# Performance work log

Measured on AMD Instinct MI355X. Metric: run time of the kernel, lower is better.

## Reference

```python
import jax, jax.numpy as jnp
import numpy as np

N = 65536
H = 1024
E = 3  # experts: SwishGLU, GEGLU, ReGLU


def setup_inputs() -> dict:
    key = jax.random.key(0)
    ks = jax.random.split(key, 10)
    s = 1.0 / np.sqrt(H)
    return {
        "x": jax.random.normal(ks[0], (N, H), jnp.float32),
        "W1": jax.random.normal(ks[1], (E, H, H), jnp.float32) * s,
        "b1": jax.random.normal(ks[2], (E, H), jnp.float32) * s,
        "W2": jax.random.normal(ks[3], (E, H, H), jnp.float32) * s,
        "b2": jax.random.normal(ks[4], (E, H), jnp.float32) * s,
        "W3": jax.random.normal(ks[5], (E, H, H), jnp.float32) * s,
        "b3": jax.random.normal(ks[6], (E, H), jnp.float32) * s,
        "Wg": jax.random.normal(ks[7], (H, E), jnp.float32) * s,
        "bg": jax.random.normal(ks[8], (E,), jnp.float32) * s,
        "gumbel_u": jax.random.uniform(ks[9], (N, E), jnp.float32),
    }


def reference(x, W1, b1, W2, b2, W3, b3, Wg, bg, gumbel_u):
    # Gate: hard gumbel-softmax (tau=1, hard=True) with straight-through estimator
    logits = x @ Wg + bg                                   # [N, E]
    u = jnp.clip(gumbel_u, 1e-6, 1.0 - 1e-6)
    g = -jnp.log(-jnp.log(u))                              # Gumbel(0,1) noise
    y_soft = jax.nn.softmax(logits + g, axis=-1)           # [N, E]
    y_hard = jax.nn.one_hot(jnp.argmax(y_soft, axis=-1), E, dtype=x.dtype)
    gate = y_hard + y_soft - jax.lax.stop_gradient(y_soft)  # values == y_hard

    # Dense compute of all three GLU experts (faithful to original module)
    h1 = jnp.einsum('nd,edh->enh', x, W1) + b1[:, None, :]  # [E, N, H]
    h3 = jnp.einsum('nd,edh->enh', x, W3) + b3[:, None, :]  # [E, N, H]
    acts = jnp.stack([
        jax.nn.silu(h1[0]),                       # SwishGLU
        jax.nn.gelu(h1[1], approximate=False),    # GEGLU (exact erf gelu)
        jax.nn.relu(h1[2]),                       # ReGLU
    ], axis=0)                                    # [E, N, H]
    inner = acts * h3                             # [E, N, H]
    out_e = jnp.einsum('end,edh->enh', inner, W2) + b2[:, None, :]  # [E, N, H]

    # Select/mix with (hard) gate weights
    return jnp.einsum('enh,ne->nh', out_e, gate)  # [N, H]
```

## Files before the change

### kernel.cpp

```cpp
#include <hip/hip_runtime.h>
#include <math.h>

#define N_TOK 65536
#define H_DIM 1024

typedef __attribute__((ext_vector_type(8))) short bf16x8;
typedef __attribute__((ext_vector_type(4))) float f32x4;

static const size_t WS_CNT   = 0;
static const size_t WS_OFFS  = 64;
static const size_t WS_PERM  = 128;
static const size_t WS_WT1   = 1ull << 20;
static const size_t WS_WT3   = WS_WT1 + 6291456ull;
static const size_t WS_WT2   = WS_WT3 + 6291456ull;
static const size_t WS_XB    = 20ull << 20;
static const size_t WS_INNER = WS_XB + 134217728ull;

static __device__ __forceinline__ unsigned short f2bf(float f) {
  union { float f; unsigned int u; } v; v.f = f;
  unsigned int r = v.u + 0x7fffu + ((v.u >> 16) & 1u);
  return (unsigned short)(r >> 16);
}

__global__ void init_kernel(int* cnt) {
  if (threadIdx.x < 4) cnt[threadIdx.x] = 0;
}

__global__ __launch_bounds__(1024) void gate_kernel(
    const float* __restrict__ x, const float* __restrict__ Wg,
    const float* __restrict__ bg, const float* __restrict__ gu,
    unsigned short* __restrict__ xb, int* __restrict__ cnt,
    int* __restrict__ perm)
{
  __shared__ float wg[3072];
  __shared__ int bexp[16];
  for (int i = threadIdx.x; i < 3072; i += 1024) wg[i] = Wg[i];
  __syncthreads();
  const int wave = threadIdx.x >> 6;
  const int lane = threadIdx.x & 63;
  const int n0 = blockIdx.x * 16;
  const int n = n0 + wave;
  const float4* xrow = (const float4*)(x + (size_t)n * H_DIM);
  unsigned short* xbrow = xb + (size_t)n * H_DIM;
  float s0 = 0.f, s1 = 0.f, s2 = 0.f;
#pragma unroll
  for (int j = 0; j < 4; j++) {
    float4 v = xrow[j * 64 + lane];
    int d0 = (j * 64 + lane) * 4;
    const float* w = &wg[d0 * 3];
    s0 += v.x * w[0] + v.y * w[3] + v.z * w[6] + v.w * w[9];
    s1 += v.x * w[1] + v.y * w[4] + v.z * w[7] + v.w * w[10];
    s2 += v.x * w[2] + v.y * w[5] + v.z * w[8] + v.w * w[11];
    uint2 p;
    p.x = (unsigned)f2bf(v.x) | ((unsigned)f2bf(v.y) << 16);
    p.y = (unsigned)f2bf(v.z) | ((unsigned)f2bf(v.w) << 16);
    ((uint2*)xbrow)[j * 64 + lane] = p;
  }
#pragma unroll
  for (int o = 32; o; o >>= 1) {
    s0 += __shfl_xor(s0, o);
    s1 += __shfl_xor(s1, o);
    s2 += __shfl_xor(s2, o);
  }
  if (lane == 0) {
    const float* u = gu + (size_t)n * 3;
    float l[3] = { s0 + bg[0], s1 + bg[1], s2 + bg[2] };
    int best = 0; float bs = -1e30f;
#pragma unroll
    for (int e = 0; e < 3; e++) {
      float uc = fminf(fmaxf(u[e], 1e-6f), 1.f - 1e-6f);
      float g = -logf(-logf(uc));
      float s = l[e] + g;
      if (s > bs) { bs = s; best = e; }
    }
    bexp[wave] = best;
  }
  __syncthreads();
  if (threadIdx.x == 0) {
    int lc[3] = {0, 0, 0};
    int lpos[16];
    for (int w = 0; w < 16; w++) lpos[w] = lc[bexp[w]]++;
    int lbase[3];
    for (int e = 0; e < 3; e++)
      lbase[e] = lc[e] ? atomicAdd(&cnt[e], lc[e]) : 0;
    for (int w = 0; w < 16; w++) {
      int e = bexp[w];
      perm[e * N_TOK + lbase[e] + lpos[w]] = n0 + w;
    }
  }
}

__global__ void offs_kernel(const int* __restrict__ cnt, int* __restrict__ offs) {
  offs[0] = 0; offs[1] = cnt[0]; offs[2] = cnt[0] + cnt[1]; offs[3] = N_TOK;
}

__global__ __launch_bounds__(256) void wcvt_kernel(
    const float* __restrict__ W1, const float* __restrict__ W3,
    const float* __restrict__ W2,
    unsigned short* __restrict__ wt1, unsigned short* __restrict__ wt3,
    unsigned short* __restrict__ wt2)
{
  const int z = blockIdx.z, e = z / 3, m = z % 3;
  const float* src = (m == 0 ? W1 : (m == 1 ? W3 : W2)) + ((size_t)e << 20);
  unsigned short* dst = (m == 0 ? wt1 : (m == 1 ? wt3 : wt2)) + ((size_t)e << 20);
  __shared__ float t[32][33];
  const int h0 = blockIdx.x * 32, d0 = blockIdx.y * 32;
  const int tx = threadIdx.x, ty = threadIdx.y;
#pragma unroll
  for (int i = 0; i < 4; i++)
    t[ty + i * 8][tx] = src[(size_t)(d0 + ty + i * 8) * H_DIM + h0 + tx];
  __syncthreads();
#pragma unroll
  for (int i = 0; i < 4; i++)
    dst[(size_t)(h0 + ty + i * 8) * H_DIM + d0 + tx] = f2bf(t[tx][ty + i * 8]);
}

__global__ __launch_bounds__(256, 2) void mlp1_kernel(
    const unsigned short* __restrict__ xb,
    const unsigned short* __restrict__ wt1,
    const unsigned short* __restrict__ wt3,
    const float* __restrict__ b1, const float* __restrict__ b3,
    const int* __restrict__ cnt, const int* __restrict__ offs,
    const int* __restrict__ perm,
    unsigned short* __restrict__ inner)
{
  const int e = blockIdx.z;
  const int ce = cnt[e];
  const int m0 = blockIdx.x * 128;
  if (m0 >= ce) return;
  const int n0 = blockIdx.y * 128;

  __shared__ short a_sh[128 * 72];
  __shared__ short p_sh[128 * 72];
  __shared__ short q_sh[128 * 72];

  const int t = threadIdx.x;
  const int br = t >> 3;
  const int c8 = (t & 7) * 8;
  const unsigned short* w1p = wt1 + ((size_t)e << 20);
  const unsigned short* w3p = wt3 + ((size_t)e << 20);

  size_t arow[4];
#pragma unroll
  for (int j = 0; j < 4; j++) {
    int r = m0 + br + 32 * j;
    int g = perm[e * N_TOK + min(r, ce - 1)];
    arow[j] = (size_t)g * H_DIM;
  }

  const int wave = t >> 6, lane = t & 63;
  const int wm = (wave & 1) * 64, wn = (wave >> 1) * 64;
  const int lr = lane & 15, quad = lane >> 4;

  f32x4 acc1[4][4], acc3[4][4];
#pragma unroll
  for (int a = 0; a < 4; a++)
#pragma unroll
    for (int b = 0; b < 4; b++) {
      acc1[a][b] = (f32x4){0.f, 0.f, 0.f, 0.f};
      acc3[a][b] = (f32x4){0.f, 0.f, 0.f, 0.f};
    }

  for (int k0 = 0; k0 < H_DIM; k0 += 64) {
    __syncthreads();
#pragma unroll
    for (int j = 0; j < 4; j++) {
      int row = br + 32 * j;
      uint4 va = *(const uint4*)(xb + arow[j] + k0 + c8);
      uint4 v1 = *(const uint4*)(w1p + (size_t)(n0 + row) * H_DIM + k0 + c8);
      uint4 v3 = *(const uint4*)(w3p + (size_t)(n0 + row) * H_DIM + k0 + c8);
      *(uint4*)&a_sh[row * 72 + c8] = va;
      *(uint4*)&p_sh[row * 72 + c8] = v1;
      *(uint4*)&q_sh[row * 72 + c8] = v3;
    }
    __syncthreads();
#pragma unroll
    for (int ks = 0; ks < 64; ks += 32) {
      bf16x8 af[4], b1f[4], b3f[4];
#pragma unroll
      for (int i = 0; i < 4; i++)
        af[i] = *(const bf16x8*)&a_sh[(wm + i * 16 + lr) * 72 + ks + quad * 8];
#pragma unroll
      for (int i = 0; i < 4; i++) {
        b1f[i] = *(const bf16x8*)&p_sh[(wn + i * 16 + lr) * 72 + ks + quad * 8];
        b3f[i] = *(const bf16x8*)&q_sh[(wn + i * 16 + lr) * 72 + ks + quad * 8];
      }
#pragma unroll
      for (int i = 0; i < 4; i++)
#pragma unroll
        for (int jn = 0; jn < 4; jn++) {
          acc1[i][jn] = __builtin_amdgcn_mfma_f32_16x16x32_bf16(af[i], b1f[jn], acc1[i][jn], 0, 0, 0);
          acc3[i][jn] = __builtin_amdgcn_mfma_f32_16x16x32_bf16(af[i], b3f[jn], acc3[i][jn], 0, 0, 0);
        }
    }
  }

  const int oe = offs[e];
#pragma unroll
  for (int jn = 0; jn < 4; jn++) {
    int col = n0 + wn + jn * 16 + lr;
    float bb1 = b1[e * H_DIM + col];
    float bb3 = b3[e * H_DIM + col];
#pragma unroll
    for (int i = 0; i < 4; i++) {
#pragma unroll
      for (int r = 0; r < 4; r++) {
        int rl = wm + i * 16 + quad * 4 + r;
        int rr = m0 + rl;
        if (rr < ce) {
          float h1 = acc1[i][jn][r] + bb1;
          float h3 = acc3[i][jn][r] + bb3;
          float a;
          if (e == 0)      a = h1 / (1.f + expf(-h1));
          else if (e == 1) a = 0.5f * h1 * (1.f + erff(h1 * 0.70710678118f));
          else             a = fmaxf(h1, 0.f);
          inner[(size_t)(oe + rr) * H_DIM + col] = f2bf(a * h3);
        }
      }
    }
  }
}

__global__ __launch_bounds__(256, 2) void mlp2_kernel(
    const unsigned short* __restrict__ inner,
    const unsigned short* __restrict__ wt2,
    const float* __restrict__ b2,
    const int* __restrict__ cnt, const int* __restrict__ offs,
    const int* __restrict__ perm,
    float* __restrict__ out)
{
  const int e = blockIdx.z;
  const int ce = cnt[e];
  const int m0 = blockIdx.x * 128;
  if (m0 >= ce) return;
  const int n0 = blockIdx.y * 128;
  const int oe = offs[e];

  __shared__ short a_sh[128 * 72];
  __shared__ short p_sh[128 * 72];

  const int t = threadIdx.x;
  const int br = t >> 3;
  const int c8 = (t & 7) * 8;
  const unsigned short* w2p = wt2 + ((size_t)e << 20);

  size_t arow[4];
#pragma unroll
  for (int j = 0; j < 4; j++) {
    int r = min(m0 + br + 32 * j, ce - 1);
    arow[j] = (size_t)(oe + r) * H_DIM;
  }

  const int wave = t >> 6, lane = t & 63;
  const int wm = (wave & 1) * 64, wn = (wave >> 1) * 64;
  const int lr = lane & 15, quad = lane >> 4;

  f32x4 acc[4][4];
#pragma unroll
  for (int a = 0; a < 4; a++)
#pragma unroll
    for (int b = 0; b < 4; b++) acc[a][b] = (f32x4){0.f, 0.f, 0.f, 0.f};

  for (int k0 = 0; k0 < H_DIM; k0 += 64) {
    __syncthreads();
#pragma unroll
    for (int j = 0; j < 4; j++) {
      int row = br + 32 * j;
      uint4 va = *(const uint4*)(inner + arow[j] + k0 + c8);
      uint4 vb = *(const uint4*)(w2p + (size_t)(n0 + row) * H_DIM + k0 + c8);
      *(uint4*)&a_sh[row * 72 + c8] = va;
      *(uint4*)&p_sh[row * 72 + c8] = vb;
    }
    __syncthreads();
#pragma unroll
    for (int ks = 0; ks < 64; ks += 32) {
      bf16x8 af[4], bf[4];
#pragma unroll
      for (int i = 0; i < 4; i++)
        af[i] = *(const bf16x8*)&a_sh[(wm + i * 16 + lr) * 72 + ks + quad * 8];
#pragma unroll
      for (int i = 0; i < 4; i++)
        bf[i] = *(const bf16x8*)&p_sh[(wn + i * 16 + lr) * 72 + ks + quad * 8];
#pragma unroll
      for (int i = 0; i < 4; i++)
#pragma unroll
        for (int jn = 0; jn < 4; jn++)
          acc[i][jn] = __builtin_amdgcn_mfma_f32_16x16x32_bf16(af[i], bf[jn], acc[i][jn], 0, 0, 0);
    }
  }

#pragma unroll
  for (int jn = 0; jn < 4; jn++) {
    int col = n0 + wn + jn * 16 + lr;
    float bb2 = b2[e * H_DIM + col];
#pragma unroll
    for (int i = 0; i < 4; i++) {
#pragma unroll
      for (int r = 0; r < 4; r++) {
        int rl = wm + i * 16 + quad * 4 + r;
        int rr = m0 + rl;
        if (rr < ce) {
          int g = perm[e * N_TOK + rr];
          out[(size_t)g * H_DIM + col] = acc[i][jn][r] + bb2;
        }
      }
    }
  }
}

extern "C" void kernel_launch(void* const* d_in, const int* in_sizes, int n_in,
                              void* d_out, int out_size, void* d_ws, size_t ws_size,
                              hipStream_t stream)
{
  const float* x  = (const float*)d_in[0];
  const float* W1 = (const float*)d_in[1];
  const float* b1 = (const float*)d_in[2];
  const float* W2 = (const float*)d_in[3];
  const float* b2 = (const float*)d_in[4];
  const float* W3 = (const float*)d_in[5];
  const float* b3 = (const float*)d_in[6];
  const float* Wg = (const float*)d_in[7];
  const float* bg = (const float*)d_in[8];
  const float* gu = (const float*)d_in[9];
  float* out = (float*)d_out;

  char* ws = (char*)d_ws;
  int* cnt  = (int*)(ws + WS_CNT);
  int* offs = (int*)(ws + WS_OFFS);
  int* perm = (int*)(ws + WS_PERM);
  unsigned short* wt1 = (unsigned short*)(ws + WS_WT1);
  unsigned short* wt3 = (unsigned short*)(ws + WS_WT3);
  unsigned short* wt2 = (unsigned short*)(ws + WS_WT2);
  unsigned short* xb  = (unsigned short*)(ws + WS_XB);
  unsigned short* inner = (unsigned short*)(ws + WS_INNER);

  init_kernel<<<1, 64, 0, stream>>>(cnt);
  gate_kernel<<<N_TOK / 16, 1024, 0, stream>>>(x, Wg, bg, gu, xb, cnt, perm);
  offs_kernel<<<1, 1, 0, stream>>>(cnt, offs);
  wcvt_kernel<<<dim3(32, 32, 9), dim3(32, 8), 0, stream>>>(W1, W3, W2, wt1, wt3, wt2);
  mlp1_kernel<<<dim3(512, 8, 3), 256, 0, stream>>>(xb, wt1, wt3, b1, b3, cnt, offs, perm, inner);
  mlp2_kernel<<<dim3(512, 8, 3), 256, 0, stream>>>(inner, wt2, b2, cnt, offs, perm, out);
}
```

Measured before the change: 1.199 ms.

## Use direct global-to-LDS loads, 32x32 MFMA tiles, and LDS-staged coalesced epilogues

Both expert GEMM kernels now fill shared memory with global_load_lds DMA instead of loading into registers and storing to LDS, and the unpadded 64-wide tiles match the DMA layout. The MFMA shape moves from 16x16x32 to 32x32x16, which needs fewer LDS fragment reads per FLOP. The epilogues stage results through LDS so the inner and output writes become 16-byte row-contiguous stores instead of scattered per-element stores. Removing the row padding may cause LDS bank conflicts on fragment reads, and the extra epilogue barriers add some synchronisation.

```diff
diff --git a/kernel.cpp b/kernel.cpp
--- a/kernel.cpp
+++ b/kernel.cpp
@@ -5,7 +5,7 @@
 #define H_DIM 1024
 
 typedef __attribute__((ext_vector_type(8))) short bf16x8;
-typedef __attribute__((ext_vector_type(4))) float f32x4;
+typedef __attribute__((ext_vector_type(16))) float f32x16;
 
 static const size_t WS_CNT   = 0;
 static const size_t WS_OFFS  = 64;
@@ -20,6 +20,12 @@
   union { float f; unsigned int u; } v; v.f = f;
   unsigned int r = v.u + 0x7fffu + ((v.u >> 16) & 1u);
   return (unsigned short)(r >> 16);
+}
+
+static __device__ __forceinline__ void lds_dma16(const void* g, void* l) {
+  __builtin_amdgcn_global_load_lds(
+      (const __attribute__((address_space(1))) unsigned int*)g,
+      (__attribute__((address_space(3))) unsigned int*)l, 16, 0, 0);
 }
 
 __global__ void init_kernel(int* cnt) {
@@ -129,94 +135,106 @@
   const int m0 = blockIdx.x * 128;
   if (m0 >= ce) return;
   const int n0 = blockIdx.y * 128;
-
-  __shared__ short a_sh[128 * 72];
-  __shared__ short p_sh[128 * 72];
-  __shared__ short q_sh[128 * 72];
+  const int oe = offs[e];
+
+  __shared__ short lds[3 * 8192];
+  short* a_sh = lds;
+  short* p_sh = lds + 8192;
+  short* q_sh = lds + 16384;
 
   const int t = threadIdx.x;
-  const int br = t >> 3;
-  const int c8 = (t & 7) * 8;
+  const int wave = t >> 6, lane = t & 63;
+  const int lrow = lane >> 3;
+  const int lk   = (lane & 7) * 8;
+
   const unsigned short* w1p = wt1 + ((size_t)e << 20);
   const unsigned short* w3p = wt3 + ((size_t)e << 20);
 
-  size_t arow[4];
-#pragma unroll
-  for (int j = 0; j < 4; j++) {
-    int r = m0 + br + 32 * j;
-    int g = perm[e * N_TOK + min(r, ce - 1)];
-    arow[j] = (size_t)g * H_DIM;
-  }
-
-  const int wave = t >> 6, lane = t & 63;
+  const unsigned short* ga[4]; const unsigned short* gb1[4]; const unsigned short* gb3[4];
+  short* la[4]; short* lp[4]; short* lq[4];
+#pragma unroll
+  for (int s = 0; s < 4; s++) {
+    int row = wave * 32 + s * 8 + lrow;
+    int g = perm[e * N_TOK + min(m0 + row, ce - 1)];
+    ga[s]  = xb  + (size_t)g * H_DIM + lk;
+    gb1[s] = w1p + (size_t)(n0 + row) * H_DIM + lk;
+    gb3[s] = w3p + (size_t)(n0 + row) * H_DIM + lk;
+    int ro = (wave * 32 + s * 8) * 64;
+    la[s] = a_sh + ro; lp[s] = p_sh + ro; lq[s] = q_sh + ro;
+  }
+
   const int wm = (wave & 1) * 64, wn = (wave >> 1) * 64;
-  const int lr = lane & 15, quad = lane >> 4;
-
-  f32x4 acc1[4][4], acc3[4][4];
-#pragma unroll
-  for (int a = 0; a < 4; a++)
-#pragma unroll
-    for (int b = 0; b < 4; b++) {
-      acc1[a][b] = (f32x4){0.f, 0.f, 0.f, 0.f};
-      acc3[a][b] = (f32x4){0.f, 0.f, 0.f, 0.f};
+  const int l31 = lane & 31, kh = lane >> 5;
+
+  f32x16 acc1[2][2], acc3[2][2];
+#pragma unroll
+  for (int a = 0; a < 2; a++)
+#pragma unroll
+    for (int b = 0; b < 2; b++) {
+      acc1[a][b] = (f32x16)(0.f);
+      acc3[a][b] = (f32x16)(0.f);
     }
 
   for (int k0 = 0; k0 < H_DIM; k0 += 64) {
     __syncthreads();
 #pragma unroll
-    for (int j = 0; j < 4; j++) {
-      int row = br + 32 * j;
-      uint4 va = *(const uint4*)(xb + arow[j] + k0 + c8);
-      uint4 v1 = *(const uint4*)(w1p + (size_t)(n0 + row) * H_DIM + k0 + c8);
-      uint4 v3 = *(const uint4*)(w3p + (size_t)(n0 + row) * H_DIM + k0 + c8);
-      *(uint4*)&a_sh[row * 72 + c8] = va;
-      *(uint4*)&p_sh[row * 72 + c8] = v1;
-      *(uint4*)&q_sh[row * 72 + c8] = v3;
-    }
-    __syncthreads();
-#pragma unroll
-    for (int ks = 0; ks < 64; ks += 32) {
-      bf16x8 af[4], b1f[4], b3f[4];
-#pragma unroll
-      for (int i = 0; i < 4; i++)
-        af[i] = *(const bf16x8*)&a_sh[(wm + i * 16 + lr) * 72 + ks + quad * 8];
-#pragma unroll
-      for (int i = 0; i < 4; i++) {
-        b1f[i] = *(const bf16x8*)&p_sh[(wn + i * 16 + lr) * 72 + ks + quad * 8];
-        b3f[i] = *(const bf16x8*)&q_sh[(wn + i * 16 + lr) * 72 + ks + quad * 8];
+    for (int s = 0; s < 4; s++) {
+      lds_dma16(ga[s] + k0, la[s]);
+      lds_dma16(gb1[s] + k0, lp[s]);
+      lds_dma16(gb3[s] + k0, lq[s]);
+    }
+    __syncthreads();
+#pragma unroll
+    for (int ks = 0; ks < 64; ks += 16) {
+      bf16x8 af[2], b1f[2], b3f[2];
+#pragma unroll
+      for (int i = 0; i < 2; i++)
+        af[i] = *(const bf16x8*)&a_sh[(wm + i * 32 + l31) * 64 + ks + kh * 8];
+#pragma unroll
+      for (int j = 0; j < 2; j++) {
+        b1f[j] = *(const bf16x8*)&p_sh[(wn + j * 32 + l31) * 64 + ks + kh * 8];
+        b3f[j] = *(const bf16x8*)&q_sh[(wn + j * 32 + l31) * 64 + ks + kh * 8];
       }
 #pragma unroll
-      for (int i = 0; i < 4; i++)
-#pragma unroll
-        for (int jn = 0; jn < 4; jn++) {
-          acc1[i][jn] = __builtin_amdgcn_mfma_f32_16x16x32_bf16(af[i], b1f[jn], acc1[i][jn], 0, 0, 0);
-          acc3[i][jn] = __builtin_amdgcn_mfma_f32_16x16x32_bf16(af[i], b3f[jn], acc3[i][jn], 0, 0, 0);
+      for (int i = 0; i < 2; i++)
+#pragma unroll
+        for (int j = 0; j < 2; j++) {
+          acc1[i][j] = __builtin_amdgcn_mfma_f32_32x32x16_bf16(af[i], b1f[j], acc1[i][j], 0, 0, 0);
+          acc3[i][j] = __builtin_amdgcn_mfma_f32_32x32x16_bf16(af[i], b3f[j], acc3[i][j], 0, 0, 0);
         }
     }
   }
 
-  const int oe = offs[e];
-#pragma unroll
-  for (int jn = 0; jn < 4; jn++) {
-    int col = n0 + wn + jn * 16 + lr;
+  __syncthreads();
+  unsigned short* C = (unsigned short*)lds;
+#pragma unroll
+  for (int j = 0; j < 2; j++) {
+    int col = n0 + wn + j * 32 + l31;
     float bb1 = b1[e * H_DIM + col];
     float bb3 = b3[e * H_DIM + col];
 #pragma unroll
-    for (int i = 0; i < 4; i++) {
-#pragma unroll
-      for (int r = 0; r < 4; r++) {
-        int rl = wm + i * 16 + quad * 4 + r;
-        int rr = m0 + rl;
-        if (rr < ce) {
-          float h1 = acc1[i][jn][r] + bb1;
-          float h3 = acc3[i][jn][r] + bb3;
-          float a;
-          if (e == 0)      a = h1 / (1.f + expf(-h1));
-          else if (e == 1) a = 0.5f * h1 * (1.f + erff(h1 * 0.70710678118f));
-          else             a = fmaxf(h1, 0.f);
-          inner[(size_t)(oe + rr) * H_DIM + col] = f2bf(a * h3);
-        }
+    for (int i = 0; i < 2; i++) {
+#pragma unroll
+      for (int reg = 0; reg < 16; reg++) {
+        int row = wm + i * 32 + (reg & 3) + 8 * (reg >> 2) + 4 * kh;
+        float h1 = acc1[i][j][reg] + bb1;
+        float h3 = acc3[i][j][reg] + bb3;
+        float a;
+        if (e == 0)      a = h1 / (1.f + expf(-h1));
+        else if (e == 1) a = 0.5f * h1 * (1.f + erff(h1 * 0.70710678118f));
+        else             a = fmaxf(h1, 0.f);
+        C[row * 128 + wn + j * 32 + l31] = f2bf(a * h3);
       }
+    }
+  }
+  __syncthreads();
+#pragma unroll
+  for (int sweep = 0; sweep < 8; sweep++) {
+    int row = sweep * 16 + (t >> 4);
+    int rr = m0 + row;
+    if (rr < ce) {
+      uint4 v = *(const uint4*)&C[row * 128 + (t & 15) * 8];
+      *(uint4*)&inner[(size_t)(oe + rr) * H_DIM + n0 + (t & 15) * 8] = v;
     }
   }
 }
@@ -236,73 +254,89 @@
   const int n0 = blockIdx.y * 128;
   const int oe = offs[e];
 
-  __shared__ short a_sh[128 * 72];
-  __shared__ short p_sh[128 * 72];
+  __shared__ short lds[2 * 8192];
+  short* a_sh = lds;
+  short* p_sh = lds + 8192;
 
   const int t = threadIdx.x;
-  const int br = t >> 3;
-  const int c8 = (t & 7) * 8;
+  const int wave = t >> 6, lane = t & 63;
+  const int lrow = lane >> 3;
+  const int lk   = (lane & 7) * 8;
   const unsigned short* w2p = wt2 + ((size_t)e << 20);
 
-  size_t arow[4];
-#pragma unroll
-  for (int j = 0; j < 4; j++) {
-    int r = min(m0 + br + 32 * j, ce - 1);
-    arow[j] = (size_t)(oe + r) * H_DIM;
-  }
-
-  const int wave = t >> 6, lane = t & 63;
+  const unsigned short* ga[4]; const unsigned short* gb[4];
+  short* la[4]; short* lp[4];
+#pragma unroll
+  for (int s = 0; s < 4; s++) {
+    int row = wave * 32 + s * 8 + lrow;
+    int r = min(m0 + row, ce - 1);
+    ga[s] = inner + (size_t)(oe + r) * H_DIM + lk;
+    gb[s] = w2p + (size_t)(n0 + row) * H_DIM + lk;
+    int ro = (wave * 32 + s * 8) * 64;
+    la[s] = a_sh + ro; lp[s] = p_sh + ro;
+  }
+
   const int wm = (wave & 1) * 64, wn = (wave >> 1) * 64;
-  const int lr = lane & 15, quad = lane >> 4;
-
-  f32x4 acc[4][4];
-#pragma unroll
-  for (int a = 0; a < 4; a++)
-#pragma unroll
-    for (int b = 0; b < 4; b++) acc[a][b] = (f32x4){0.f, 0.f, 0.f, 0.f};
+  const int l31 = lane & 31, kh = lane >> 5;
+
+  f32x16 acc[2][2];
+#pragma unroll
+  for (int a = 0; a < 2; a++)
+#pragma unroll
+    for (int b = 0; b < 2; b++) acc[a][b] = (f32x16)(0.f);
 
   for (int k0 = 0; k0 < H_DIM; k0 += 64) {
     __syncthreads();
 #pragma unroll
-    for (int j = 0; j < 4; j++) {
-      int row = br + 32 * j;
-      uint4 va = *(const uint4*)(inner + arow[j] + k0 + c8);
-      uint4 vb = *(const uint4*)(w2p + (size_t)(n0 + row) * H_DIM + k0 + c8);
-      *(uint4*)&a_sh[row * 72 + c8] = va;
-      *(uint4*)&p_sh[row * 72 + c8] = vb;
-    }
-    __syncthreads();
-#pragma unroll
-    for (int ks = 0; ks < 64; ks += 32) {
-      bf16x8 af[4], bf[4];
-#pragma unroll
-      for (int i = 0; i < 4; i++)
-        af[i] = *(const bf16x8*)&a_sh[(wm + i * 16 + lr) * 72 + ks + quad * 8];
-#pragma unroll
-      for (int i = 0; i < 4; i++)
-        bf[i] = *(const bf16x8*)&p_sh[(wn + i * 16 + lr) * 72 + ks + quad * 8];
-#pragma unroll
-      for (int i = 0; i < 4; i++)
-#pragma unroll
-        for (int jn = 0; jn < 4; jn++)
-          acc[i][jn] = __builtin_amdgcn_mfma_f32_16x16x32_bf16(af[i], bf[jn], acc[i][jn], 0, 0, 0);
-    }
-  }
-
-#pragma unroll
-  for (int jn = 0; jn < 4; jn++) {
-    int col = n0 + wn + jn * 16 + lr;
-    float bb2 = b2[e * H_DIM + col];
-#pragma unroll
-    for (int i = 0; i < 4; i++) {
-#pragma unroll
-      for (int r = 0; r < 4; r++) {
-        int rl = wm + i * 16 + quad * 4 + r;
-        int rr = m0 + rl;
-        if (rr < ce) {
-          int g = perm[e * N_TOK + rr];
-          out[(size_t)g * H_DIM + col] = acc[i][jn][r] + bb2;
+    for (int s = 0; s < 4; s++) {
+      lds_dma16(ga[s] + k0, la[s]);
+      lds_dma16(gb[s] + k0, lp[s]);
+    }
+    __syncthreads();
+#pragma unroll
+    for (int ks = 0; ks < 64; ks += 16) {
+      bf16x8 af[2], bf[2];
+#pragma unroll
+      for (int i = 0; i < 2; i++)
+        af[i] = *(const bf16x8*)&a_sh[(wm + i * 32 + l31) * 64 + ks + kh * 8];
+#pragma unroll
+      for (int j = 0; j < 2; j++)
+        bf[j] = *(const bf16x8*)&p_sh[(wn + j * 32 + l31) * 64 + ks + kh * 8];
+#pragma unroll
+      for (int i = 0; i < 2; i++)
+#pragma unroll
+        for (int j = 0; j < 2; j++)
+          acc[i][j] = __builtin_amdgcn_mfma_f32_32x32x16_bf16(af[i], bf[j], acc[i][j], 0, 0, 0);
+    }
+  }
+
+  float* C = (float*)lds;
+#pragma unroll
+  for (int half = 0; half < 2; half++) {
+    __syncthreads();
+    if ((wave & 1) == half) {
+#pragma unroll
+      for (int j = 0; j < 2; j++) {
+        float bb2 = b2[e * H_DIM + n0 + wn + j * 32 + l31];
+#pragma unroll
+        for (int i = 0; i < 2; i++) {
+#pragma unroll
+          for (int reg = 0; reg < 16; reg++) {
+            int row = i * 32 + (reg & 3) + 8 * (reg >> 2) + 4 * kh;
+            C[row * 128 + wn + j * 32 + l31] = acc[i][j][reg] + bb2;
+          }
         }
+      }
+    }
+    __syncthreads();
+#pragma unroll
+    for (int sweep = 0; sweep < 8; sweep++) {
+      int row = sweep * 8 + (t >> 5);
+      int rr = m0 + half * 64 + row;
+      if (rr < ce) {
+        int g = perm[e * N_TOK + rr];
+        uint4 v = *(const uint4*)&C[row * 128 + (t & 31) * 4];
+        *(uint4*)&out[(size_t)g * H_DIM + n0 + (t & 31) * 4] = v;
       }
     }
   }
```

Result: slower. 1.354 ms (+13.0%).
